# Optimization experiments

Hardware: AMD Instinct MI355X
Metric: run time of the kernel (lower is better)

## Reference

```python
import jax, jax.numpy as jnp
import numpy as np

MIN_DISTANCE = 2.9
LOSS_WEIGHT = 1.0

def setup_inputs() -> dict:
    key = jax.random.key(0)
    coordinates = jax.random.normal(key, (64, 3072), dtype=jnp.float32) * 5.0
    return {"coordinates": coordinates}

def reference(coordinates) -> jnp.ndarray:
    B, C = coordinates.shape
    N = C // 3
    atoms = coordinates.reshape(B, N, 3)
    # pairwise squared distances: [B, N, N]
    diff = atoms[:, :, None, :] - atoms[:, None, :, :]
    dist_sq = jnp.sum(diff * diff, axis=-1)
    dist = jnp.sqrt(dist_sq + 1e-8)
    # strict upper-triangular mask (i < j), same for every batch element
    i = jnp.arange(N)
    triu = (i[:, None] < i[None, :]).astype(dist.dtype)  # [N, N]
    violations = jnp.maximum(MIN_DISTANCE - dist, 0.0) * triu
    total_loss = jnp.sum(violations * violations)
    return LOSS_WEIGHT * total_loss / B
```

## Files before the change

kernel.cpp:

```cpp
#include <hip/hip_runtime.h>


constexpr int   NA    = 1024;
constexpr int   JCH   = 256;
constexpr float MIN_D = 2.9f;

__global__ __launch_bounds__(256, 4)
void collapse_loss_kernel(const float* __restrict__ coords,
                          float* __restrict__ out)
{
    const int b   = blockIdx.x;
    const int ic  = blockIdx.y;
    const int jc  = blockIdx.z;
    const int tid = threadIdx.x;

    __shared__ float sx[JCH], sy[JCH], sz[JCH];

    const float* cb = coords + (size_t)b * (NA * 3);
    const int jbase = jc * JCH;

    {
        const int ja = jbase + tid;
        sx[tid] = cb[3 * ja + 0];
        sy[tid] = cb[3 * ja + 1];
        sz[tid] = cb[3 * ja + 2];
    }

    const int i = ic * 256 + tid;
    const float xi = cb[3 * i + 0];
    const float yi = cb[3 * i + 1];
    const float zi = cb[3 * i + 2];

    __syncthreads();

    float acc = 0.0f;
    #pragma unroll 8
    for (int j = 0; j < JCH; ++j) {
        const float dx = xi - sx[j];
        const float dy = yi - sy[j];
        const float dz = zi - sz[j];
        float ds = fmaf(dx, dx, fmaf(dy, dy, dz * dz)) + 1e-8f;
        float d  = __builtin_amdgcn_sqrtf(ds);
        float v  = fmaxf(MIN_D - d, 0.0f);
        float c  = v * v;
        if (i == jbase + j) c = 0.0f;
        acc += c;
    }

    #pragma unroll
    for (int off = 1; off < 64; off <<= 1)
        acc += __shfl_xor(acc, off, 64);

    __shared__ float wsum[4];
    if ((tid & 63) == 0) wsum[tid >> 6] = acc;
    __syncthreads();
    if (tid == 0) {
        const float s = (wsum[0] + wsum[1]) + (wsum[2] + wsum[3]);
        atomicAdd(out, s * (0.5f / 64.0f));
    }
}

extern "C" void kernel_launch(void* const* d_in, const int* in_sizes, int n_in,
                              void* d_out, int out_size, void* d_ws, size_t ws_size,
                              hipStream_t stream)
{
    const float* coords = (const float*)d_in[0];
    float* out = (float*)d_out;

    hipMemsetAsync(out, 0, sizeof(float) * out_size, stream);

    dim3 grid(64, NA / 256, NA / JCH);
    collapse_loss_kernel<<<grid, 256, 0, stream>>>(coords, out);
}
```

Before: 82.14 us.

## Drop diagonal mask, two atoms per thread, partials buffer with separate reduce kernel

Measured after the change: 74.00 us. 1.11x faster.

```diff
diff --git a/kernel.cpp b/kernel.cpp
--- a/kernel.cpp
+++ b/kernel.cpp
@@ -1,62 +1,94 @@
 #include <hip/hip_runtime.h>
 
 
-constexpr int   NA    = 1024;
-constexpr int   JCH   = 256;
-constexpr float MIN_D = 2.9f;
+constexpr int   NA      = 1024;
+constexpr int   NB      = 64;
+constexpr int   JCH     = 128;
+constexpr int   THREADS = 256;
+constexpr int   IPT     = 2;
+constexpr int   ICH     = THREADS * IPT;
+constexpr int   GRID_I  = NA / ICH;
+constexpr int   GRID_J  = NA / JCH;
+constexpr int   NPART   = NB * GRID_I * GRID_J;
+constexpr float MIN_D   = 2.9f;
 
-__global__ __launch_bounds__(256, 4)
-void collapse_loss_kernel(const float* __restrict__ coords,
-                          float* __restrict__ out)
+__global__ __launch_bounds__(THREADS, 4)
+void pair_kernel(const float* __restrict__ coords, float* __restrict__ partials)
 {
     const int b   = blockIdx.x;
     const int ic  = blockIdx.y;
     const int jc  = blockIdx.z;
     const int tid = threadIdx.x;
 
-    __shared__ float sx[JCH], sy[JCH], sz[JCH];
+    __shared__ float sj[JCH * 3];
 
     const float* cb = coords + (size_t)b * (NA * 3);
-    const int jbase = jc * JCH;
+    const float* cj = cb + jc * (JCH * 3);
 
-    {
-        const int ja = jbase + tid;
-        sx[tid] = cb[3 * ja + 0];
-        sy[tid] = cb[3 * ja + 1];
-        sz[tid] = cb[3 * ja + 2];
-    }
+    sj[tid] = cj[tid];
+    if (tid < JCH * 3 - THREADS) sj[THREADS + tid] = cj[THREADS + tid];
 
-    const int i = ic * 256 + tid;
-    const float xi = cb[3 * i + 0];
-    const float yi = cb[3 * i + 1];
-    const float zi = cb[3 * i + 2];
+    const int i0 = ic * ICH + tid;
+    const int i1 = i0 + THREADS;
+    const float x0 = cb[3*i0+0], y0 = cb[3*i0+1], z0 = cb[3*i0+2];
+    const float x1 = cb[3*i1+0], y1 = cb[3*i1+1], z1 = cb[3*i1+2];
 
     __syncthreads();
 
-    float acc = 0.0f;
+    float acc0 = 0.f, acc1 = 0.f;
     #pragma unroll 8
     for (int j = 0; j < JCH; ++j) {
-        const float dx = xi - sx[j];
-        const float dy = yi - sy[j];
-        const float dz = zi - sz[j];
-        float ds = fmaf(dx, dx, fmaf(dy, dy, dz * dz)) + 1e-8f;
-        float d  = __builtin_amdgcn_sqrtf(ds);
-        float v  = fmaxf(MIN_D - d, 0.0f);
-        float c  = v * v;
-        if (i == jbase + j) c = 0.0f;
-        acc += c;
+        const float xj = sj[3*j+0], yj = sj[3*j+1], zj = sj[3*j+2];
+        {
+            const float dx = x0-xj, dy = y0-yj, dz = z0-zj;
+            const float ds = fmaf(dx,dx, fmaf(dy,dy, fmaf(dz,dz, 1e-8f)));
+            const float v  = fmaxf(MIN_D - __builtin_amdgcn_sqrtf(ds), 0.f);
+            acc0 = fmaf(v, v, acc0);
+        }
+        {
+            const float dx = x1-xj, dy = y1-yj, dz = z1-zj;
+            const float ds = fmaf(dx,dx, fmaf(dy,dy, fmaf(dz,dz, 1e-8f)));
+            const float v  = fmaxf(MIN_D - __builtin_amdgcn_sqrtf(ds), 0.f);
+            acc1 = fmaf(v, v, acc1);
+        }
     }
+    float acc = acc0 + acc1;
 
     #pragma unroll
     for (int off = 1; off < 64; off <<= 1)
         acc += __shfl_xor(acc, off, 64);
 
-    __shared__ float wsum[4];
+    __shared__ float wsum[THREADS / 64];
     if ((tid & 63) == 0) wsum[tid >> 6] = acc;
     __syncthreads();
     if (tid == 0) {
-        const float s = (wsum[0] + wsum[1]) + (wsum[2] + wsum[3]);
-        atomicAdd(out, s * (0.5f / 64.0f));
+        float s = 0.f;
+        #pragma unroll
+        for (int w = 0; w < THREADS / 64; ++w) s += wsum[w];
+        partials[(b * GRID_I + ic) * GRID_J + jc] = s;
+    }
+}
+
+__global__ __launch_bounds__(256)
+void reduce_kernel(const float* __restrict__ partials, float* __restrict__ out)
+{
+    const int tid = threadIdx.x;
+    float s = 0.f;
+    #pragma unroll
+    for (int k = tid; k < NPART; k += 256) s += partials[k];
+    #pragma unroll
+    for (int off = 1; off < 64; off <<= 1)
+        s += __shfl_xor(s, off, 64);
+    __shared__ float wsum[4];
+    if ((tid & 63) == 0) wsum[tid >> 6] = s;
+    __syncthreads();
+    if (tid == 0) {
+        float tot = (wsum[0] + wsum[1]) + (wsum[2] + wsum[3]);
+        const float d0 = __builtin_amdgcn_sqrtf(1e-8f);
+        const float v0 = fmaxf(MIN_D - d0, 0.f);
+        const float cd = v0 * v0;
+        tot -= (float)(NB * NA) * cd;
+        out[0] = tot * (0.5f / (float)NB);
     }
 }
 
@@ -65,10 +97,10 @@
                               hipStream_t stream)
 {
     const float* coords = (const float*)d_in[0];
+    float* partials = (float*)d_ws;
     float* out = (float*)d_out;
 
-    hipMemsetAsync(out, 0, sizeof(float) * out_size, stream);
-
-    dim3 grid(64, NA / 256, NA / JCH);
-    collapse_loss_kernel<<<grid, 256, 0, stream>>>(coords, out);
+    dim3 grid(NB, GRID_I, GRID_J);
+    pair_kernel<<<grid, THREADS, 0, stream>>>(coords, partials);
+    reduce_kernel<<<1, 256, 0, stream>>>(partials, out);
 }
```
